# Kernel tuning notes

Measured on AMD Instinct MI355X. Metric: run time of the kernel, lower is better.

The kernel has to match this reference:

```python
import jax, jax.numpy as jnp
import numpy as np

# RReLU in eval mode == leaky relu with slope (lower+upper)/2
_SLOPE = (0.001 + 0.004) / 2.0  # 0.0025

def _rrelu(x):
    return jnp.where(x >= 0, x, _SLOPE * x)

_DIMS = [(8, 8), (8, 4), (4, 4), (4, 4), (4, 4), (4, 4), (4, 1),
         (1, 4), (4, 4), (4, 4), (4, 4), (4, 4), (4, 8)]
_NAMES = ['in', 'h1', 'h2', 'h3', 'h4', 'h5', 'encode',
          'h6', 'h7', 'h8', 'h9', 'h10', 'decode']


def setup_inputs() -> dict:
    key = jax.random.key(0)
    keys = jax.random.split(key, 1 + 2 * len(_DIMS))
    inp = {'x_in': jax.random.normal(keys[0], (4194304, 8), dtype=jnp.float32)}
    for i, (name, (fi, fo)) in enumerate(zip(_NAMES, _DIMS)):
        bound = 1.0 / np.sqrt(fi)
        inp[f'W_{name}'] = jax.random.uniform(keys[1 + 2 * i], (fi, fo),
                                              minval=-bound, maxval=bound,
                                              dtype=jnp.float32)
        inp[f'b_{name}'] = jax.random.uniform(keys[2 + 2 * i], (fo,),
                                              minval=-bound, maxval=bound,
                                              dtype=jnp.float32)
    return inp


def reference(x_in, W_in, b_in, W_h1, b_h1, W_h2, b_h2, W_h3, b_h3,
              W_h4, b_h4, W_h5, b_h5, W_encode, b_encode, W_h6, b_h6,
              W_h7, b_h7, W_h8, b_h8, W_h9, b_h9, W_h10, b_h10,
              W_decode, b_decode):
    lin = lambda x, W, b: x @ W + b
    x = x_in  # (x - mean)/std with mean=0, std=1 is identity
    x = lin(_rrelu(lin(x, W_in, b_in)), W_h1, b_h1)
    x = x + lin(_rrelu(lin(x, W_h2, b_h2)), W_h3, b_h3)
    x = x + lin(_rrelu(lin(x, W_h4, b_h4)), W_h5, b_h5)
    x_encode = _rrelu(lin(x, W_encode, b_encode))
    x = _rrelu(lin(x_encode, W_h6, b_h6))
    x = x + lin(_rrelu(lin(x, W_h7, b_h7)), W_h8, b_h8)
    x = x + lin(_rrelu(lin(x, W_h9, b_h9)), W_h10, b_h10)
    x_decode = _rrelu(lin(x, W_decode, b_decode))
    return (x_encode, x_decode)
```

## Files before the change

### kernel.cpp

```cpp
#include <hip/hip_runtime.h>

#define N_ROWS 4194304
#define RPT 4
#define BLOCK 256

enum : int {
    O_W_in = 0,    O_b_in = 64,
    O_W_h1 = 72,   O_b_h1 = 104,
    O_W_h2 = 108,  O_b_h2 = 124,
    O_W_h3 = 128,  O_b_h3 = 144,
    O_W_h4 = 148,  O_b_h4 = 164,
    O_W_h5 = 168,  O_b_h5 = 184,
    O_W_enc = 188, O_b_enc = 192,
    O_W_h6 = 193,  O_b_h6 = 197,
    O_W_h7 = 201,  O_b_h7 = 217,
    O_W_h8 = 221,  O_b_h8 = 237,
    O_W_h9 = 241,  O_b_h9 = 257,
    O_W_h10 = 261, O_b_h10 = 277,
    O_W_dec = 281, O_b_dec = 313,
    W_TOTAL = 321
};

__device__ __forceinline__ float rrelu(float v) {
    return fmaxf(v, 0.0025f * v);
}

__device__ __forceinline__ void resblock(float x[RPT][4],
                                         const float* __restrict__ Wa,
                                         const float* __restrict__ ba,
                                         const float* __restrict__ Wb,
                                         const float* __restrict__ bb) {
    float t[RPT][4];
#pragma unroll
    for (int j = 0; j < 4; ++j) {
#pragma unroll
        for (int k = 0; k < RPT; ++k) {
            float acc = ba[j];
#pragma unroll
            for (int i = 0; i < 4; ++i) acc = fmaf(x[k][i], Wa[i * 4 + j], acc);
            t[k][j] = rrelu(acc);
        }
    }
#pragma unroll
    for (int j = 0; j < 4; ++j) {
#pragma unroll
        for (int k = 0; k < RPT; ++k) {
            float acc = bb[j];
#pragma unroll
            for (int i = 0; i < 4; ++i) acc = fmaf(t[k][i], Wb[i * 4 + j], acc);
            x[k][j] += acc;
        }
    }
}

__global__ __launch_bounds__(BLOCK) void ann_fused_kernel(
    const float* __restrict__ x_in, const float* __restrict__ wf,
    float* __restrict__ out) {
    const int tid = blockIdx.x * BLOCK + threadIdx.x;
    const int T = N_ROWS / RPT;

    float xin[RPT][8];
#pragma unroll
    for (int k = 0; k < RPT; ++k) {
        const float4* p =
            reinterpret_cast<const float4*>(x_in + (size_t)(tid + k * T) * 8);
        float4 a = p[0], b = p[1];
        xin[k][0] = a.x; xin[k][1] = a.y; xin[k][2] = a.z; xin[k][3] = a.w;
        xin[k][4] = b.x; xin[k][5] = b.y; xin[k][6] = b.z; xin[k][7] = b.w;
    }

    float t8[RPT][8];
#pragma unroll
    for (int j = 0; j < 8; ++j) {
#pragma unroll
        for (int k = 0; k < RPT; ++k) {
            float acc = wf[O_b_in + j];
#pragma unroll
            for (int i = 0; i < 8; ++i)
                acc = fmaf(xin[k][i], wf[O_W_in + i * 8 + j], acc);
            t8[k][j] = rrelu(acc);
        }
    }

    float x[RPT][4];
#pragma unroll
    for (int j = 0; j < 4; ++j) {
#pragma unroll
        for (int k = 0; k < RPT; ++k) {
            float acc = wf[O_b_h1 + j];
#pragma unroll
            for (int i = 0; i < 8; ++i)
                acc = fmaf(t8[k][i], wf[O_W_h1 + i * 4 + j], acc);
            x[k][j] = acc;
        }
    }

    resblock(x, wf + O_W_h2, wf + O_b_h2, wf + O_W_h3, wf + O_b_h3);
    resblock(x, wf + O_W_h4, wf + O_b_h4, wf + O_W_h5, wf + O_b_h5);

    float e[RPT];
#pragma unroll
    for (int k = 0; k < RPT; ++k) {
        float acc = wf[O_b_enc];
#pragma unroll
        for (int i = 0; i < 4; ++i) acc = fmaf(x[k][i], wf[O_W_enc + i], acc);
        e[k] = rrelu(acc);
    }

#pragma unroll
    for (int j = 0; j < 4; ++j) {
#pragma unroll
        for (int k = 0; k < RPT; ++k) {
            x[k][j] = rrelu(fmaf(e[k], wf[O_W_h6 + j], wf[O_b_h6 + j]));
        }
    }

    resblock(x, wf + O_W_h7, wf + O_b_h7, wf + O_W_h8, wf + O_b_h8);
    resblock(x, wf + O_W_h9, wf + O_b_h9, wf + O_W_h10, wf + O_b_h10);

    float d[RPT][8];
#pragma unroll
    for (int j = 0; j < 8; ++j) {
#pragma unroll
        for (int k = 0; k < RPT; ++k) {
            float acc = wf[O_b_dec + j];
#pragma unroll
            for (int i = 0; i < 4; ++i)
                acc = fmaf(x[k][i], wf[O_W_dec + i * 8 + j], acc);
            d[k][j] = rrelu(acc);
        }
    }

#pragma unroll
    for (int k = 0; k < RPT; ++k) {
        const int row = tid + k * T;
        out[row] = e[k];
        float4* q = reinterpret_cast<float4*>(out + N_ROWS + (size_t)row * 8);
        q[0] = make_float4(d[k][0], d[k][1], d[k][2], d[k][3]);
        q[1] = make_float4(d[k][4], d[k][5], d[k][6], d[k][7]);
    }
}

extern "C" void kernel_launch(void* const* d_in, const int* in_sizes, int n_in,
                              void* d_out, int out_size, void* d_ws, size_t ws_size,
                              hipStream_t stream) {
    const float* x_in = (const float*)d_in[0];
    float* wf = (float*)d_ws;

    static const int sz[26] = {64, 8, 32, 4, 16, 4, 16, 4, 16, 4, 16, 4,
                               4,  1, 4,  4, 16, 4, 16, 4, 16, 4, 16, 4, 32, 8};
    int off = 0;
    for (int i = 0; i < 26; ++i) {
        hipMemcpyAsync(wf + off, d_in[1 + i], sz[i] * sizeof(float),
                       hipMemcpyDeviceToDevice, stream);
        off += sz[i];
    }

    float* out = (float*)d_out;
    const int total_threads = N_ROWS / RPT;
    dim3 grid(total_threads / BLOCK), block(BLOCK);
    ann_fused_kernel<<<grid, block, 0, stream>>>(x_in, wf, out);
}
```

Measured before the change: 354.7 us.

## Replace per-tensor weight memcpys with a pack kernel and vectorize weight loads

Result: faster. 316.5 us (-10.8%).

```diff
diff --git a/kernel.cpp b/kernel.cpp
--- a/kernel.cpp
+++ b/kernel.cpp
@@ -12,45 +12,86 @@
     O_W_h4 = 148,  O_b_h4 = 164,
     O_W_h5 = 168,  O_b_h5 = 184,
     O_W_enc = 188, O_b_enc = 192,
-    O_W_h6 = 193,  O_b_h6 = 197,
-    O_W_h7 = 201,  O_b_h7 = 217,
-    O_W_h8 = 221,  O_b_h8 = 237,
-    O_W_h9 = 241,  O_b_h9 = 257,
-    O_W_h10 = 261, O_b_h10 = 277,
-    O_W_dec = 281, O_b_dec = 313,
-    W_TOTAL = 321
+    O_W_h6 = 196,  O_b_h6 = 200,
+    O_W_h7 = 204,  O_b_h7 = 220,
+    O_W_h8 = 224,  O_b_h8 = 240,
+    O_W_h9 = 244,  O_b_h9 = 260,
+    O_W_h10 = 264, O_b_h10 = 280,
+    O_W_dec = 284, O_b_dec = 316,
+    W_TOTAL = 324
 };
 
 __device__ __forceinline__ float rrelu(float v) {
     return fmaxf(v, 0.0025f * v);
 }
 
-__device__ __forceinline__ void resblock(float x[RPT][4],
-                                         const float* __restrict__ Wa,
-                                         const float* __restrict__ ba,
-                                         const float* __restrict__ Wb,
-                                         const float* __restrict__ bb) {
-    float t[RPT][4];
+template <int FI, int FO, bool RELU>
+__device__ __forceinline__ void lin(const float* __restrict__ wf, int Woff,
+                                    int boff, const float (&x)[RPT][FI],
+                                    float (&y)[RPT][FO]) {
 #pragma unroll
-    for (int j = 0; j < 4; ++j) {
+    for (int jg = 0; jg < FO; jg += 4) {
+        float4 b4 = *reinterpret_cast<const float4*>(wf + boff + jg);
+        float acc[RPT][4];
 #pragma unroll
         for (int k = 0; k < RPT; ++k) {
-            float acc = ba[j];
+            acc[k][0] = b4.x; acc[k][1] = b4.y;
+            acc[k][2] = b4.z; acc[k][3] = b4.w;
+        }
 #pragma unroll
-            for (int i = 0; i < 4; ++i) acc = fmaf(x[k][i], Wa[i * 4 + j], acc);
-            t[k][j] = rrelu(acc);
+        for (int i = 0; i < FI; ++i) {
+            float4 w4 = *reinterpret_cast<const float4*>(wf + Woff + i * FO + jg);
+            float wa[4] = {w4.x, w4.y, w4.z, w4.w};
+#pragma unroll
+            for (int k = 0; k < RPT; ++k)
+#pragma unroll
+                for (int c = 0; c < 4; ++c)
+                    acc[k][c] = fmaf(x[k][i], wa[c], acc[k][c]);
         }
+#pragma unroll
+        for (int k = 0; k < RPT; ++k)
+#pragma unroll
+            for (int c = 0; c < 4; ++c)
+                y[k][jg + c] = RELU ? rrelu(acc[k][c]) : acc[k][c];
     }
+}
+
+template <int FI, int FO>
+__device__ __forceinline__ void lin_add(const float* __restrict__ wf, int Woff,
+                                        int boff, const float (&x)[RPT][FI],
+                                        float (&y)[RPT][FO]) {
 #pragma unroll
-    for (int j = 0; j < 4; ++j) {
+    for (int jg = 0; jg < FO; jg += 4) {
+        float4 b4 = *reinterpret_cast<const float4*>(wf + boff + jg);
+        float acc[RPT][4];
 #pragma unroll
         for (int k = 0; k < RPT; ++k) {
-            float acc = bb[j];
+            acc[k][0] = b4.x; acc[k][1] = b4.y;
+            acc[k][2] = b4.z; acc[k][3] = b4.w;
+        }
 #pragma unroll
-            for (int i = 0; i < 4; ++i) acc = fmaf(t[k][i], Wb[i * 4 + j], acc);
-            x[k][j] += acc;
+        for (int i = 0; i < FI; ++i) {
+            float4 w4 = *reinterpret_cast<const float4*>(wf + Woff + i * FO + jg);
+            float wa[4] = {w4.x, w4.y, w4.z, w4.w};
+#pragma unroll
+            for (int k = 0; k < RPT; ++k)
+#pragma unroll
+                for (int c = 0; c < 4; ++c)
+                    acc[k][c] = fmaf(x[k][i], wa[c], acc[k][c]);
         }
+#pragma unroll
+        for (int k = 0; k < RPT; ++k)
+#pragma unroll
+            for (int c = 0; c < 4; ++c) y[k][jg + c] += acc[k][c];
     }
+}
+
+__device__ __forceinline__ void resblock(const float* __restrict__ wf, int Oa,
+                                         int Oba, int Ob, int Obb,
+                                         float (&x)[RPT][4]) {
+    float t[RPT][4];
+    lin<4, 4, true>(wf, Oa, Oba, x, t);
+    lin_add<4, 4>(wf, Ob, Obb, t, x);
 }
 
 __global__ __launch_bounds__(BLOCK) void ann_fused_kernel(
@@ -70,66 +111,40 @@
     }
 
     float t8[RPT][8];
-#pragma unroll
-    for (int j = 0; j < 8; ++j) {
-#pragma unroll
-        for (int k = 0; k < RPT; ++k) {
-            float acc = wf[O_b_in + j];
-#pragma unroll
-            for (int i = 0; i < 8; ++i)
-                acc = fmaf(xin[k][i], wf[O_W_in + i * 8 + j], acc);
-            t8[k][j] = rrelu(acc);
-        }
-    }
+    lin<8, 8, true>(wf, O_W_in, O_b_in, xin, t8);
+    float x[RPT][4];
+    lin<8, 4, false>(wf, O_W_h1, O_b_h1, t8, x);
 
-    float x[RPT][4];
-#pragma unroll
-    for (int j = 0; j < 4; ++j) {
-#pragma unroll
-        for (int k = 0; k < RPT; ++k) {
-            float acc = wf[O_b_h1 + j];
-#pragma unroll
-            for (int i = 0; i < 8; ++i)
-                acc = fmaf(t8[k][i], wf[O_W_h1 + i * 4 + j], acc);
-            x[k][j] = acc;
-        }
-    }
+    resblock(wf, O_W_h2, O_b_h2, O_W_h3, O_b_h3, x);
+    resblock(wf, O_W_h4, O_b_h4, O_W_h5, O_b_h5, x);
 
-    resblock(x, wf + O_W_h2, wf + O_b_h2, wf + O_W_h3, wf + O_b_h3);
-    resblock(x, wf + O_W_h4, wf + O_b_h4, wf + O_W_h5, wf + O_b_h5);
-
+    float4 we = *reinterpret_cast<const float4*>(wf + O_W_enc);
+    float be = wf[O_b_enc];
     float e[RPT];
 #pragma unroll
     for (int k = 0; k < RPT; ++k) {
-        float acc = wf[O_b_enc];
-#pragma unroll
-        for (int i = 0; i < 4; ++i) acc = fmaf(x[k][i], wf[O_W_enc + i], acc);
-        e[k] = rrelu(acc);
+        float a = fmaf(x[k][0], we.x, be);
+        a = fmaf(x[k][1], we.y, a);
+        a = fmaf(x[k][2], we.z, a);
+        a = fmaf(x[k][3], we.w, a);
+        e[k] = rrelu(a);
     }
 
+    float4 w6 = *reinterpret_cast<const float4*>(wf + O_W_h6);
+    float4 b6 = *reinterpret_cast<const float4*>(wf + O_b_h6);
 #pragma unroll
-    for (int j = 0; j < 4; ++j) {
-#pragma unroll
-        for (int k = 0; k < RPT; ++k) {
-            x[k][j] = rrelu(fmaf(e[k], wf[O_W_h6 + j], wf[O_b_h6 + j]));
-        }
+    for (int k = 0; k < RPT; ++k) {
+        x[k][0] = rrelu(fmaf(e[k], w6.x, b6.x));
+        x[k][1] = rrelu(fmaf(e[k], w6.y, b6.y));
+        x[k][2] = rrelu(fmaf(e[k], w6.z, b6.z));
+        x[k][3] = rrelu(fmaf(e[k], w6.w, b6.w));
     }
 
-    resblock(x, wf + O_W_h7, wf + O_b_h7, wf + O_W_h8, wf + O_b_h8);
-    resblock(x, wf + O_W_h9, wf + O_b_h9, wf + O_W_h10, wf + O_b_h10);
+    resblock(wf, O_W_h7, O_b_h7, O_W_h8, O_b_h8, x);
+    resblock(wf, O_W_h9, O_b_h9, O_W_h10, O_b_h10, x);
 
     float d[RPT][8];
-#pragma unroll
-    for (int j = 0; j < 8; ++j) {
-#pragma unroll
-        for (int k = 0; k < RPT; ++k) {
-            float acc = wf[O_b_dec + j];
-#pragma unroll
-            for (int i = 0; i < 4; ++i)
-                acc = fmaf(x[k][i], wf[O_W_dec + i * 8 + j], acc);
-            d[k][j] = rrelu(acc);
-        }
-    }
+    lin<4, 8, true>(wf, O_W_dec, O_b_dec, x, d);
 
 #pragma unroll
     for (int k = 0; k < RPT; ++k) {
@@ -141,20 +156,31 @@
     }
 }
 
+struct SrcPtrs { const float* p[26]; };
+
+__global__ void pack_weights(SrcPtrs s, float* __restrict__ wf) {
+    const int t = threadIdx.x;
+    const int off[26] = {O_W_in,  O_b_in,  O_W_h1,  O_b_h1,  O_W_h2, O_b_h2,
+                         O_W_h3,  O_b_h3,  O_W_h4,  O_b_h4,  O_W_h5, O_b_h5,
+                         O_W_enc, O_b_enc, O_W_h6,  O_b_h6,  O_W_h7, O_b_h7,
+                         O_W_h8,  O_b_h8,  O_W_h9,  O_b_h9,  O_W_h10,
+                         O_b_h10, O_W_dec, O_b_dec};
+    const int sz[26] = {64, 8, 32, 4, 16, 4, 16, 4, 16, 4, 16, 4, 4,
+                        1,  4, 4,  16, 4, 16, 4, 16, 4, 16, 4, 32, 8};
+#pragma unroll 1
+    for (int g = 0; g < 26; ++g)
+        if (t < sz[g]) wf[off[g] + t] = s.p[g][t];
+}
+
 extern "C" void kernel_launch(void* const* d_in, const int* in_sizes, int n_in,
                               void* d_out, int out_size, void* d_ws, size_t ws_size,
                               hipStream_t stream) {
     const float* x_in = (const float*)d_in[0];
     float* wf = (float*)d_ws;
 
-    static const int sz[26] = {64, 8, 32, 4, 16, 4, 16, 4, 16, 4, 16, 4,
-                               4,  1, 4,  4, 16, 4, 16, 4, 16, 4, 16, 4, 32, 8};
-    int off = 0;
-    for (int i = 0; i < 26; ++i) {
-        hipMemcpyAsync(wf + off, d_in[1 + i], sz[i] * sizeof(float),
-                       hipMemcpyDeviceToDevice, stream);
-        off += sz[i];
-    }
+    SrcPtrs s;
+    for (int i = 0; i < 26; ++i) s.p[i] = (const float*)d_in[1 + i];
+    pack_weights<<<1, 64, 0, stream>>>(s, wf);
 
     float* out = (float*)d_out;
     const int total_threads = N_ROWS / RPT;
```
